# Performance work log

Hardware: AMD Instinct MI355X
Metric: run time of the kernel (lower is better)

Reference implementation:

```python
import jax, jax.numpy as jnp
import numpy as np

D_MODEL = 1024
NUM_HEADS = 16
HEAD_DIM = D_MODEL // NUM_HEADS  # 64
SCALE = HEAD_DIM ** -0.5
BIAS_LEN = 128  # min(max_seq_len=512, 128)
ROPE_BASE = 10000.0
LN_EPS = 1e-5


def setup_inputs() -> dict:
    key = jax.random.key(0)
    ks = jax.random.split(key, 8)
    B, Lq, Lkv = 8, 512, 512
    return {
        "decoder_hidden": jax.random.normal(ks[0], (B, Lq, D_MODEL), jnp.float32),
        "encoder_output": jax.random.normal(ks[1], (B, Lkv, D_MODEL), jnp.float32),
        "Wqkv": jax.random.normal(ks[2], (3 * D_MODEL, D_MODEL), jnp.float32) * 0.02,
        "Wout": jax.random.normal(ks[3], (D_MODEL, D_MODEL), jnp.float32) * 0.02,
        "b_out": jnp.zeros((D_MODEL,), jnp.float32),
        "Wgate": jax.random.normal(ks[4], (D_MODEL, D_MODEL), jnp.float32) * 0.02,
        "b_gate": jnp.zeros((D_MODEL,), jnp.float32),
        "gamma": jnp.ones((D_MODEL,), jnp.float32),
        "beta": jnp.zeros((D_MODEL,), jnp.float32),
    }


def _layernorm(x, gamma, beta):
    mu = jnp.mean(x, axis=-1, keepdims=True)
    var = jnp.mean(jnp.square(x - mu), axis=-1, keepdims=True)
    return (x - mu) * jax.lax.rsqrt(var + LN_EPS) * gamma + beta


def _rope(x, cos, sin):
    # x: [B, H, L, HEAD_DIM]; cos/sin: [L, HEAD_DIM//2]
    half = HEAD_DIM // 2
    c = cos[None, None, :, :]
    s = sin[None, None, :, :]
    x_even, x_odd = x[..., :half], x[..., half:]
    return jnp.concatenate([x_even * c - x_odd * s, x_even * s + x_odd * c], axis=-1)


def _temporal_bias(L_q, L_kv):
    pos = jnp.arange(BIAS_LEN, dtype=jnp.float32)
    dist = jnp.abs(pos[None, :] - pos[:, None])  # [128,128]
    bias = jnp.exp(-dist * 0.1) - dist * 0.05
    if L_q <= BIAS_LEN and L_kv <= BIAS_LEN:
        return bias[:L_q, :L_kv]
    # bilinear interpolation (align_corners=False / half-pixel) fallback
    return jax.image.resize(bias, (L_q, L_kv), method="bilinear")


def reference(decoder_hidden, encoder_output, Wqkv, Wout, b_out, Wgate, b_gate, gamma, beta):
    B, L_q, _ = decoder_hidden.shape
    L_kv = encoder_output.shape[1]
    residual = decoder_hidden

    q_in = _layernorm(decoder_hidden, gamma, beta)
    kv_in = _layernorm(encoder_output, gamma, beta)

    q = q_in @ Wqkv[:D_MODEL].T
    k = kv_in @ Wqkv[D_MODEL:2 * D_MODEL].T
    v = kv_in @ Wqkv[2 * D_MODEL:].T

    q = q.reshape(B, L_q, NUM_HEADS, HEAD_DIM).transpose(0, 2, 1, 3)
    k = k.reshape(B, L_kv, NUM_HEADS, HEAD_DIM).transpose(0, 2, 1, 3)
    v = v.reshape(B, L_kv, NUM_HEADS, HEAD_DIM).transpose(0, 2, 1, 3)

    # rotary embedding over max(L_q, L_kv) positions
    L = max(L_q, L_kv)
    inv_freq = 1.0 / ROPE_BASE ** (jnp.arange(0, HEAD_DIM, 2, dtype=jnp.float32) / HEAD_DIM)
    freqs = jnp.arange(L, dtype=jnp.float32)[:, None] * inv_freq[None, :]  # [L, HEAD_DIM//2]
    cos, sin = jnp.cos(freqs), jnp.sin(freqs)
    q = _rope(q, cos[:L_q], sin[:L_q])
    k = _rope(k, cos[:L_kv], sin[:L_kv])

    scores = jnp.einsum("bhqd,bhkd->bhqk", q, k) * SCALE
    scores = scores + _temporal_bias(L_q, L_kv)[None, None, :, :]

    attn = jax.nn.softmax(scores, axis=-1)
    attended = jnp.einsum("bhqk,bhkd->bhqd", attn, v)
    attended = attended.transpose(0, 2, 1, 3).reshape(B, L_q, D_MODEL)
    attended = attended @ Wout.T + b_out

    gate = jax.nn.sigmoid(attended @ Wgate.T + b_gate)
    output = gate * attended + (1.0 - gate) * residual
    return output
```

## Files before the change

kernel.cpp:

```cpp
#include <hip/hip_runtime.h>
#include <hip/hip_bf16.h>

#define D_MODEL 1024
#define NHEADS 16
#define HDIM 64
#define BATCH 8
#define SEQ 512
#define NROWS 4096
#define SCALE 0.125f
#define LN_EPS 1e-5f

typedef __attribute__((ext_vector_type(8))) short bf16x8;
typedef __attribute__((ext_vector_type(4))) float f32x4;
typedef __attribute__((ext_vector_type(8))) unsigned short u16x8;

static __device__ __forceinline__ float bf2f(unsigned short u) {
    return __uint_as_float(((unsigned int)u) << 16);
}
static __device__ __forceinline__ unsigned short f2bf(float f) {
    unsigned int x = __float_as_uint(f);
    unsigned int r = (x + 0x7fffu + ((x >> 16) & 1u)) >> 16;
    return (unsigned short)r;
}

#define GLOAD16(gp, lp)                                                        \
    __builtin_amdgcn_global_load_lds(                                          \
        (const __attribute__((address_space(1))) void*)(gp),                   \
        (__attribute__((address_space(3))) void*)(lp), 16, 0, 0)

#define VMW(n) asm volatile("s_waitcnt vmcnt(" #n ")" ::: "memory")
#define RBAR() __builtin_amdgcn_s_barrier()

static __device__ __forceinline__ float bias128(int a, int b) {
    float d = fabsf((float)(a - b));
    return expf(-d * 0.1f) - d * 0.05f;
}

__global__ void prep_kernel(const float* __restrict__ dec, const float* __restrict__ enc,
                            const float* __restrict__ gamma, const float* __restrict__ beta,
                            const float* __restrict__ Wqkv,
                            const float* __restrict__ Wout, const float* __restrict__ Wgate,
                            unsigned short* __restrict__ q_ln, unsigned short* __restrict__ kv_ln,
                            float* __restrict__ bias, unsigned short* __restrict__ Wqkv_bf,
                            unsigned short* __restrict__ Wout_bf, unsigned short* __restrict__ Wgate_bf) {
    int blk = blockIdx.x;
    int t = threadIdx.x;
    if (blk >= 12288) {
        int idx = (blk - 12288) * 256 + t;
        const float* src; unsigned short* dst; int off;
        if (idx < 262144) { src = Wout; dst = Wout_bf; off = idx; }
        else              { src = Wgate; dst = Wgate_bf; off = idx - 262144; }
        float4 v = ((const float4*)src)[off];
        ushort4 u;
        u.x = f2bf(v.x); u.y = f2bf(v.y); u.z = f2bf(v.z); u.w = f2bf(v.w);
        ((ushort4*)dst)[off] = u;
        return;
    }
    if (blk >= 9216) {
        int idx = (blk - 9216) * 256 + t;
        float4 v = ((const float4*)Wqkv)[idx];
        ushort4 u;
        u.x = f2bf(v.x); u.y = f2bf(v.y); u.z = f2bf(v.z); u.w = f2bf(v.w);
        ((ushort4*)Wqkv_bf)[idx] = u;
        return;
    }
    if (blk >= 8192) {
        int idx = (blk - 8192) * 256 + t;
        int qi = idx >> 9, kj = idx & 511;
        float fq = (qi + 0.5f) * 0.25f - 0.5f;
        float fk = (kj + 0.5f) * 0.25f - 0.5f;
        int iq = (int)floorf(fq); float tq = fq - (float)iq;
        int ik = (int)floorf(fk); float tk = fk - (float)ik;
        int iq0 = min(max(iq, 0), 127), iq1 = min(max(iq + 1, 0), 127);
        int ik0 = min(max(ik, 0), 127), ik1 = min(max(ik + 1, 0), 127);
        float v = (1.f - tq) * ((1.f - tk) * bias128(iq0, ik0) + tk * bias128(iq0, ik1))
                +        tq  * ((1.f - tk) * bias128(iq1, ik0) + tk * bias128(iq1, ik1));
        bias[idx] = v;
        return;
    }
    int row = blk;
    const float* src = (row < NROWS) ? dec + (size_t)row * D_MODEL
                                     : enc + (size_t)(row - NROWS) * D_MODEL;
    unsigned short* dst = (row < NROWS) ? q_ln + (size_t)row * D_MODEL
                                        : kv_ln + (size_t)(row - NROWS) * D_MODEL;
    float4 x = ((const float4*)src)[t];
    float s  = x.x + x.y + x.z + x.w;
    float ss = x.x * x.x + x.y * x.y + x.z * x.z + x.w * x.w;
    #pragma unroll
    for (int off = 32; off > 0; off >>= 1) {
        s  += __shfl_down(s, off);
        ss += __shfl_down(ss, off);
    }
    __shared__ float red_s[4], red_ss[4];
    int wid = t >> 6, lane = t & 63;
    if (lane == 0) { red_s[wid] = s; red_ss[wid] = ss; }
    __syncthreads();
    if (t == 0) {
        float S = red_s[0] + red_s[1] + red_s[2] + red_s[3];
        float SS = red_ss[0] + red_ss[1] + red_ss[2] + red_ss[3];
        red_s[0] = S; red_ss[0] = SS;
    }
    __syncthreads();
    float mu  = red_s[0] * (1.0f / 1024.0f);
    float var = red_ss[0] * (1.0f / 1024.0f) - mu * mu;
    float rstd = rsqrtf(var + LN_EPS);
    float4 g = ((const float4*)gamma)[t];
    float4 bb = ((const float4*)beta)[t];
    ushort4 u;
    u.x = f2bf((x.x - mu) * rstd * g.x + bb.x);
    u.y = f2bf((x.y - mu) * rstd * g.y + bb.y);
    u.z = f2bf((x.z - mu) * rstd * g.z + bb.z);
    u.w = f2bf((x.w - mu) * rstd * g.w + bb.w);
    ((ushort4*)dst)[t] = u;
}

__global__ void convert_og(const float* __restrict__ Wout, const float* __restrict__ Wgate,
                           unsigned short* __restrict__ Wout_bf, unsigned short* __restrict__ Wgate_bf) {
    int idx = blockIdx.x * 256 + threadIdx.x;
    const float* src; unsigned short* dst; int off;
    if (idx < 262144) { src = (const float*)Wout; dst = Wout_bf; off = idx; }
    else              { src = (const float*)Wgate; dst = Wgate_bf; off = idx - 262144; }
    float4 v = ((const float4*)src)[off];
    ushort4 u;
    u.x = f2bf(v.x); u.y = f2bf(v.y); u.z = f2bf(v.z); u.w = f2bf(v.w);
    ((ushort4*)dst)[off] = u;
}

#define CSTR 136

struct alignas(16) Smem64B {
    unsigned short A[64 * 128];
    unsigned short B[128 * 128];
};

#define MF(a, b, d) __builtin_amdgcn_mfma_f32_16x16x32_bf16((a), (b), (d), 0, 0, 0)

#define GEMM_KH2B(kh)                                                          \
    {                                                                          \
        int pofs = (((kh) * 4 + quad) ^ c) * 8;                                \
        const unsigned short* Arow_ = &As2[(wr * 32 + c) * 128 + pofs];        \
        const unsigned short* Brow_ = &Bs2[(wc * 64 + c) * 128 + pofs];        \
        bf16x8 f0 = *(const bf16x8*)(Arow_);                                   \
        bf16x8 f1 = *(const bf16x8*)(Arow_ + 2048);                            \
        bf16x8 g0 = *(const bf16x8*)(Brow_);                                   \
        bf16x8 g1 = *(const bf16x8*)(Brow_ + 2048);                            \
        bf16x8 g2 = *(const bf16x8*)(Brow_ + 4096);                            \
        bf16x8 g3 = *(const bf16x8*)(Brow_ + 6144);                            \
        c00 = MF(f0, g0, c00); c01 = MF(f0, g1, c01); c02 = MF(f0, g2, c02); c03 = MF(f0, g3, c03); \
        c10 = MF(f1, g0, c10); c11 = MF(f1, g1, c11); c12 = MF(f1, g2, c12); c13 = MF(f1, g3, c13); \
    }

#define GEMM_BODY_64B(Aptr, Bptr)                                              \
    int wave = tid >> 6, lane = tid & 63, quad = lane >> 4, c = lane & 15;     \
    int wr = wave >> 1, wc = wave & 1;                                         \
    int l4 = lane >> 4, l15 = lane & 15;                                       \
    const unsigned short* Abase = (Aptr) + (size_t)(rt * 64) * 1024;           \
    const unsigned short* Bbase = (Bptr) + (size_t)(ct * 128) * 1024;          \
    int aoff0 = (wave * 16 +  0 + l4) * 1024 + ((l15 ^ ( 0 + l4)) * 8);        \
    int aoff1 = (wave * 16 +  4 + l4) * 1024 + ((l15 ^ ( 4 + l4)) * 8);        \
    int aoff2 = (wave * 16 +  8 + l4) * 1024 + ((l15 ^ ( 8 + l4)) * 8);        \
    int aoff3 = (wave * 16 + 12 + l4) * 1024 + ((l15 ^ (12 + l4)) * 8);        \
    int boff0 = (wave * 32 +  0 + l4) * 1024 + ((l15 ^ (( 0 + l4) & 15)) * 8); \
    int boff1 = (wave * 32 +  4 + l4) * 1024 + ((l15 ^ (( 4 + l4) & 15)) * 8); \
    int boff2 = (wave * 32 +  8 + l4) * 1024 + ((l15 ^ (( 8 + l4) & 15)) * 8); \
    int boff3 = (wave * 32 + 12 + l4) * 1024 + ((l15 ^ ((12 + l4) & 15)) * 8); \
    int boff4 = (wave * 32 + 16 + l4) * 1024 + ((l15 ^ ((16 + l4) & 15)) * 8); \
    int boff5 = (wave * 32 + 20 + l4) * 1024 + ((l15 ^ ((20 + l4) & 15)) * 8); \
    int boff6 = (wave * 32 + 24 + l4) * 1024 + ((l15 ^ ((24 + l4) & 15)) * 8); \
    int boff7 = (wave * 32 + 28 + l4) * 1024 + ((l15 ^ ((28 + l4) & 15)) * 8); \
    unsigned short* AsW = As2 + wave * 2048;                                   \
    unsigned short* BsW = Bs2 + wave * 4096;                                   \
    f32x4 c00 = (f32x4)0.f, c01 = (f32x4)0.f, c02 = (f32x4)0.f, c03 = (f32x4)0.f; \
    f32x4 c10 = (f32x4)0.f, c11 = (f32x4)0.f, c12 = (f32x4)0.f, c13 = (f32x4)0.f; \
    for (int kt = 0; kt < 8; ++kt) {                                           \
        int k0 = kt * 128;                                                     \
        __syncthreads();                                                       \
        GLOAD16(Abase + aoff0 + k0, AsW);                                      \
        GLOAD16(Abase + aoff1 + k0, AsW + 512);                                \
        GLOAD16(Abase + aoff2 + k0, AsW + 1024);                               \
        GLOAD16(Abase + aoff3 + k0, AsW + 1536);                               \
        GLOAD16(Bbase + boff0 + k0, BsW);                                      \
        GLOAD16(Bbase + boff1 + k0, BsW + 512);                                \
        GLOAD16(Bbase + boff2 + k0, BsW + 1024);                               \
        GLOAD16(Bbase + boff3 + k0, BsW + 1536);                               \
        GLOAD16(Bbase + boff4 + k0, BsW + 2048);                               \
        GLOAD16(Bbase + boff5 + k0, BsW + 2560);                               \
        GLOAD16(Bbase + boff6 + k0, BsW + 3072);                               \
        GLOAD16(Bbase + boff7 + k0, BsW + 3584);                               \
        __syncthreads();                                                       \
        GEMM_KH2B(0)                                                           \
        GEMM_KH2B(1)                                                           \
        GEMM_KH2B(2)                                                           \
        GEMM_KH2B(3)                                                           \
    }

union alignas(16) SmemQS {
    struct { unsigned short A[64 * 64]; unsigned short B[128 * 64]; } ab;
    unsigned short C[64 * CSTR];
    unsigned short Ct[128 * 72];
};

#define QKH(pA, pB, kh)                                                        \
    {                                                                          \
        int pofs = (((kh) * 4 + quad) ^ x7) * 8;                               \
        const unsigned short* Ar_ = (pA) + (wr * 32 + c) * 64 + pofs;          \
        const unsigned short* Br_ = (pB) + (wc * 64 + c) * 64 + pofs;          \
        bf16x8 f0 = *(const bf16x8*)(Ar_);                                     \
        bf16x8 f1 = *(const bf16x8*)(Ar_ + 1024);                              \
        bf16x8 g0 = *(const bf16x8*)(Br_);                                     \
        bf16x8 g1 = *(const bf16x8*)(Br_ + 1024);                              \
        bf16x8 g2 = *(const bf16x8*)(Br_ + 2048);                              \
        bf16x8 g3 = *(const bf16x8*)(Br_ + 3072);                              \
        c00 = MF(f0, g0, c00); c01 = MF(f0, g1, c01); c02 = MF(f0, g2, c02); c03 = MF(f0, g3, c03); \
        c10 = MF(f1, g0, c10); c11 = MF(f1, g1, c11); c12 = MF(f1, g2, c12); c13 = MF(f1, g3, c13); \
    }

#define QROPE_REG(i, reg, A0, A1, A2, A3)                                      \
    {                                                                          \
        int mloc = wr * 32 + (i) * 16 + quad * 4 + (reg);                      \
        int crow = mloc * CSTR + wc * 64;                                      \
        float fl = (float)((rt * 64 + mloc) & 511);                            \
        float aa0 = fl * inv0, aa1 = fl * inv1;                                \
        float c0 = cosf(aa0), s0 = sinf(aa0);                                  \
        float c1 = cosf(aa1), s1 = sinf(aa1);                                  \
        float e0 = A0[(reg)], o0 = A2[(reg)];                                  \
        float e1 = A1[(reg)], o1 = A3[(reg)];                                  \
        smemq.C[crow + c]      = f2bf(e0 * c0 - o0 * s0);                      \
        smemq.C[crow + 32 + c] = f2bf(e0 * s0 + o0 * c0);                      \
        smemq.C[crow + 16 + c] = f2bf(e1 * c1 - o1 * s1);                      \
        smemq.C[crow + 48 + c] = f2bf(e1 * s1 + o1 * c1);                      \
    }
#define QROPE_ROW(i, A0, A1, A2, A3)                                           \
    QROPE_REG(i, 0, A0, A1, A2, A3) QROPE_REG(i, 1, A0, A1, A2, A3)            \
    QROPE_REG(i, 2, A0, A1, A2, A3) QROPE_REG(i, 3, A0, A1, A2, A3)

#define QVSECT_REG(i, j, reg, Acc)                                             \
    smemq.Ct[(wc * 64 + (j) * 16 + c) * 72 + (wr * 32 + (i) * 16 + quad * 4 + (reg))] = f2bf(Acc[(reg)]);
#define QVSECT_TILE(i, j, Acc)                                                 \
    QVSECT_REG(i, j, 0, Acc) QVSECT_REG(i, j, 1, Acc)                          \
    QVSECT_REG(i, j, 2, Acc) QVSECT_REG(i, j, 3, Acc)

__global__ __launch_bounds__(256, 6)
void qkv_gemm_mfma(const unsigned short* __restrict__ q_ln,
                   const unsigned short* __restrict__ kv_ln,
                   const unsigned short* __restrict__ Wb,
                   unsigned short* __restrict__ qo,
                   unsigned short* __restrict__ ko,
                   unsigned short* __restrict__ vo) {
    int bid = blockIdx.x;
    int wg = (bid & 7) * 192 + (bid >> 3);
    int st = wg >> 5, in = wg & 31;
    int stc = st >> 4, str = st & 15;
    int ct = stc * 8 + (in & 7);
    int rt = str * 4 + (in >> 3);
    int n0 = ct * 128;
    int section = stc;
    const unsigned short* A = (section == 0) ? q_ln : kv_ln;

    __shared__ SmemQS smemq;
    unsigned short* As2 = smemq.ab.A;
    unsigned short* Bs2 = smemq.ab.B;
    int tid = threadIdx.x;
    int wave = tid >> 6, lane = tid & 63, quad = lane >> 4, c = lane & 15;
    int wr = wave >> 1, wc = wave & 1;
    int x7 = c & 7;

    int soff = (tid >> 3) * 1024 + (((tid & 7) ^ ((tid >> 3) & 7)) * 8);
    const unsigned short* Ab = A + (size_t)(rt * 64) * 1024 + soff;
    const unsigned short* Bb = Wb + (size_t)n0 * 1024 + soff;
    int stW = wave * 512;

    f32x4 c00 = (f32x4)0.f, c01 = (f32x4)0.f, c02 = (f32x4)0.f, c03 = (f32x4)0.f;
    f32x4 c10 = (f32x4)0.f, c11 = (f32x4)0.f, c12 = (f32x4)0.f, c13 = (f32x4)0.f;

    for (int kt = 0; kt < 16; ++kt) {
        int k0 = kt * 64;
        __syncthreads();
        GLOAD16(Ab + k0,          As2 + stW);
        GLOAD16(Ab + 32768 + k0,  As2 + stW + 2048);
        GLOAD16(Bb + k0,          Bs2 + stW);
        GLOAD16(Bb + 32768 + k0,  Bs2 + stW + 2048);
        GLOAD16(Bb + 65536 + k0,  Bs2 + stW + 4096);
        GLOAD16(Bb + 98304 + k0,  Bs2 + stW + 6144);
        __syncthreads();
        QKH(As2, Bs2, 0)
        QKH(As2, Bs2, 1)
    }

    __syncthreads();

    if (section == 2) {
        QVSECT_TILE(0, 0, c00) QVSECT_TILE(0, 1, c01) QVSECT_TILE(0, 2, c02) QVSECT_TILE(0, 3, c03)
        QVSECT_TILE(1, 0, c10) QVSECT_TILE(1, 1, c11) QVSECT_TILE(1, 2, c12) QVSECT_TILE(1, 3, c13)
        __syncthreads();
        int dr = tid >> 1, hh = tid & 1;
        int h = ((n0 & 1023) >> 6) + (dr >> 6);
        int d = dr & 63;
        int mmb = rt * 64;
        int bb = mmb >> 9, ll0 = mmb & 511;
        unsigned short* orow = vo + (((size_t)bb * NHEADS + h) * HDIM + d) * SEQ + ll0 + hh * 32;
        const unsigned short* csrc = &smemq.Ct[dr * 72 + hh * 32];
        #pragma unroll
        for (int kc = 0; kc < 4; ++kc)
            *(u16x8*)(orow + kc * 8) = *(const u16x8*)(csrc + kc * 8);
        return;
    }

    float inv0 = expf(-0.2878231366f * (float)c);
    float inv1 = expf(-0.2878231366f * (float)(16 + c));
    QROPE_ROW(0, c00, c01, c02, c03)
    QROPE_ROW(1, c10, c11, c12, c13)
    __syncthreads();

    unsigned short* outp = (section == 0) ? qo : ko;
    int rr = tid >> 2;
    int ch = (tid >> 1) & 1;
    int sub = tid & 1;
    int mm = rt * 64 + rr;
    int bb = mm >> 9, ll = mm & 511;
    int h = ((n0 & 1023) >> 6) + ch;
    unsigned short* orow = outp + (((size_t)bb * NHEADS + h) * SEQ + ll) * HDIM + sub * 32;
    const unsigned short* csrc = &smemq.C[rr * CSTR + ch * 64 + sub * 32];
    #pragma unroll
    for (int kc = 0; kc < 4; ++kc)
        *(u16x8*)(orow + kc * 8) = *(const u16x8*)(csrc + kc * 8);
}

#define O1_REG(mb, reg, n, Acc)                                                \
    t_bf[(size_t)((mb) + (reg)) * 1024 + (n)] = f2bf(Acc[(reg)] + bo);
#define O1_TILE(i, j, Acc)                                                     \
    {                                                                          \
        int n = ct * 128 + wc * 64 + (j) * 16 + c;                             \
        float bo = b_out[n];                                                   \
        int mb = rt * 64 + wr * 32 + (i) * 16 + quad * 4;                      \
        O1_REG(mb, 0, n, Acc) O1_REG(mb, 1, n, Acc)                            \
        O1_REG(mb, 2, n, Acc) O1_REG(mb, 3, n, Acc)                            \
    }

__global__ __launch_bounds__(256, 1)
void out_gemm1_mfma(const unsigned short* __restrict__ att,
                    const unsigned short* __restrict__ Wob,
                    const float* __restrict__ b_out,
                    unsigned short* __restrict__ t_bf) {
    int ct = blockIdx.x, rt = blockIdx.y;
    __shared__ Smem64B smem2;
    unsigned short* As2 = smem2.A;
    unsigned short* Bs2 = smem2.B;
    int tid = threadIdx.x;

    GEMM_BODY_64B(att, Wob)

    O1_TILE(0, 0, c00) O1_TILE(0, 1, c01) O1_TILE(0, 2, c02) O1_TILE(0, 3, c03)
    O1_TILE(1, 0, c10) O1_TILE(1, 1, c11) O1_TILE(1, 2, c12) O1_TILE(1, 3, c13)
}

#define O2_REG(mb, reg, n, Acc)                                                \
    {                                                                          \
        float gz = Acc[(reg)] + bg;                                            \
        float g = 1.0f / (1.0f + expf(-gz));                                   \
        size_t idx = (size_t)((mb) + (reg)) * 1024 + (n);                      \
        float tv = bf2f(t_bf[idx]);                                            \
        float rv = residual[idx];                                              \
        out[idx] = g * tv + (1.0f - g) * rv;                                   \
    }
#define O2_TILE(i, j, Acc)                                                     \
    {                                                                          \
        int n = ct * 128 + wc * 64 + (j) * 16 + c;                             \
        float bg = b_gate[n];                                                  \
        int mb = rt * 64 + wr * 32 + (i) * 16 + quad * 4;                      \
        O2_REG(mb, 0, n, Acc) O2_REG(mb, 1, n, Acc)                            \
        O2_REG(mb, 2, n, Acc) O2_REG(mb, 3, n, Acc)                            \
    }

__global__ __launch_bounds__(256, 1)
void out_gemm2_mfma(const unsigned short* __restrict__ t_bf,
                    const unsigned short* __restrict__ Wgb,
                    const float* __restrict__ b_gate,
                    const float* __restrict__ residual,
                    float* __restrict__ out) {
    int ct = blockIdx.x, rt = blockIdx.y;
    __shared__ Smem64B smem2;
    unsigned short* As2 = smem2.A;
    unsigned short* Bs2 = smem2.B;
    int tid = threadIdx.x;

    GEMM_BODY_64B(t_bf, Wgb)

    O2_TILE(0, 0, c00) O2_TILE(0, 1, c01) O2_TILE(0, 2, c02) O2_TILE(0, 3, c03)
    O2_TILE(1, 0, c10) O2_TILE(1, 1, c11) O2_TILE(1, 2, c12) O2_TILE(1, 3, c13)
}

#define KSTR 72

static __device__ __forceinline__ void attn_step(
    const unsigned short* __restrict__ KsB, const unsigned short* __restrict__ VsB,
    int kv0, const float* __restrict__ bias, unsigned short* __restrict__ Ps,
    int q0, int wb, int quad, int c, int p0, int p1,
    bf16x8 aq0, bf16x8 aq1, f32x4 (&oacc)[4], float (&lrow)[4])
{
    f32x4 sacc[4];
    #pragma unroll
    for (int nt = 0; nt < 4; ++nt) {
        const unsigned short* kbase = &KsB[(nt * 16 + c) * 64];
        bf16x8 b0 = *(const bf16x8*)(kbase + p0);
        bf16x8 b1 = *(const bf16x8*)(kbase + p1);
        f32x4 a = (f32x4)0.f;
        a = __builtin_amdgcn_mfma_f32_16x16x32_bf16(aq0, b0, a, 0, 0, 0);
        a = __builtin_amdgcn_mfma_f32_16x16x32_bf16(aq1, b1, a, 0, 0, 0);
        sacc[nt] = a;
    }
    const float* bbase = bias + (size_t)(q0 + wb + quad * 4) * 512 + kv0 + c;
    float tsum[4];
    #pragma unroll
    for (int r = 0; r < 4; ++r) tsum[r] = 0.f;
    #pragma unroll
    for (int nt = 0; nt < 4; ++nt)
        #pragma unroll
        for (int r = 0; r < 4; ++r) {
            float p = __expf(sacc[nt][r] * SCALE + bbase[(size_t)r * 512 + nt * 16]);
            tsum[r] += p;
            Ps[(wb + quad * 4 + r) * KSTR + nt * 16 + c] = f2bf(p);
        }
    #pragma unroll
    for (int r = 0; r < 4; ++r) {
        float t = tsum[r];
        t += __shfl_xor(t, 1);
        t += __shfl_xor(t, 2);
        t += __shfl_xor(t, 4);
        t += __shfl_xor(t, 8);
        lrow[r] += t;
    }
    bf16x8 pb0 = *(const bf16x8*)&Ps[(wb + c) * KSTR + quad * 8];
    bf16x8 pb1 = *(const bf16x8*)&Ps[(wb + c) * KSTR + 32 + quad * 8];
    #pragma unroll
    for (int t = 0; t < 4; ++t) {
        const unsigned short* vbase = &VsB[(t * 16 + c) * 64];
        bf16x8 a0 = *(const bf16x8*)(vbase + p0);
        bf16x8 a1 = *(const bf16x8*)(vbase + p1);
        oacc[t] = __builtin_amdgcn_mfma_f32_16x16x32_bf16(a0, pb0, oacc[t], 0, 0, 0);
        oacc[t] = __builtin_amdgcn_mfma_f32_16x16x32_bf16(a1, pb1, oacc[t], 0, 0, 0);
    }
}

#define ASTAGE(BUF, kvt)                                                       \
    GLOAD16(kgb + (size_t)((kvt) * 64) * HDIM, Ks[BUF] + wave * 512);          \
    GLOAD16(vgb + (kvt) * 64, Vs[BUF] + wave * 512);

__global__ __launch_bounds__(512)
void attn_kernel(const unsigned short* __restrict__ q,
                 const unsigned short* __restrict__ k,
                 const unsigned short* __restrict__ vt,
                 const float* __restrict__ bias,
                 unsigned short* __restrict__ attended) {
    int qt = blockIdx.x, h = blockIdx.y, b = blockIdx.z;
    __shared__ unsigned short Ks[2][64 * 64];
    __shared__ unsigned short Vs[2][64 * 64];
    __shared__ unsigned short Ps[128 * KSTR];
    __shared__ float lf[128];

    int tid = threadIdx.x;
    int wave = tid >> 6, lane = tid & 63;
    int quad = lane >> 4, c = lane & 15;
    int wb = wave * 16;
    size_t headbase = (((size_t)b * NHEADS + h) * SEQ) * HDIM;
    int q0 = qt * 128;

    const unsigned short* qrow = q + headbase + (size_t)(q0 + wb + c) * HDIM;
    bf16x8 aq0 = *(const bf16x8*)(qrow + quad * 8);
    bf16x8 aq1 = *(const bf16x8*)(qrow + 32 + quad * 8);

    int srow = wave * 8 + (lane >> 3);
    int schunk = (lane & 7) ^ (srow & 7);
    const unsigned short* kgb = k + headbase + (size_t)srow * HDIM + schunk * 8;
    const unsigned short* vgb = vt + headbase + (size_t)srow * SEQ + schunk * 8;
    int x7 = c & 7;
    int p0 = (quad ^ x7) * 8;
    int p1 = ((4 + quad) ^ x7) * 8;

    f32x4 oacc[4];
    #pragma unroll
    for (int t = 0; t < 4; ++t) oacc[t] = (f32x4)0.f;
    float lrow[4];
    #pragma unroll
    for (int r = 0; r < 4; ++r) lrow[r] = 0.f;

    ASTAGE(0, 0)
    ASTAGE(1, 1)
    VMW(2); RBAR();
    for (int kt2 = 0; kt2 < 4; ++kt2) {
        attn_step(Ks[0], Vs[0], (kt2 * 2) * 64, bias, Ps,
                  q0, wb, quad, c, p0, p1, aq0, aq1, oacc, lrow);
        RBAR();
        if (kt2 < 3) { ASTAGE(0, kt2 * 2 + 2) VMW(2); }
        else         { VMW(0); }
        RBAR();
        attn_step(Ks[1], Vs[1], (kt2 * 2 + 1) * 64, bias, Ps,
                  q0, wb, quad, c, p0, p1, aq0, aq1, oacc, lrow);
        RBAR();
        if (kt2 < 3) { ASTAGE(1, kt2 * 2 + 3) VMW(2); }
        RBAR();
    }

    if (c == 0) {
        f32x4 lv;
        lv[0] = lrow[0]; lv[1] = lrow[1]; lv[2] = lrow[2]; lv[3] = lrow[3];
        *(f32x4*)&lf[wb + quad * 4] = lv;
    }
    float invl = 1.0f / lf[wb + c];
    unsigned short* drow = attended + ((size_t)b * SEQ + (q0 + wb + c)) * D_MODEL + h * HDIM;
    #pragma unroll
    for (int t = 0; t < 4; ++t) {
        ushort4 o;
        o.x = f2bf(oacc[t][0] * invl);
        o.y = f2bf(oacc[t][1] * invl);
        o.z = f2bf(oacc[t][2] * invl);
        o.w = f2bf(oacc[t][3] * invl);
        *(ushort4*)(drow + t * 16 + quad * 4) = o;
    }
}

extern "C" void kernel_launch(void* const* d_in, const int* in_sizes, int n_in,
                              void* d_out, int out_size, void* d_ws, size_t ws_size,
                              hipStream_t stream) {
    const float* dec    = (const float*)d_in[0];
    const float* enc    = (const float*)d_in[1];
    const float* Wqkv   = (const float*)d_in[2];
    const float* Wout   = (const float*)d_in[3];
    const float* b_out  = (const float*)d_in[4];
    const float* Wgate  = (const float*)d_in[5];
    const float* b_gate = (const float*)d_in[6];
    const float* gamma  = (const float*)d_in[7];
    const float* beta   = (const float*)d_in[8];
    float* out = (float*)d_out;

    char* ws = (char*)d_ws;
    const size_t MB = 1024 * 1024;
    unsigned short* q_ln    = (unsigned short*)(ws + 0 * MB);
    unsigned short* kv_ln   = (unsigned short*)(ws + 8 * MB);
    unsigned short* qb      = (unsigned short*)(ws + 16 * MB);
    unsigned short* kb      = (unsigned short*)(ws + 24 * MB);
    unsigned short* vb      = (unsigned short*)(ws + 32 * MB);
    unsigned short* Wqkv_bf = (unsigned short*)(ws + 40 * MB);
    float*          bias    = (float*)(ws + 46 * MB);
    unsigned short* att     = (unsigned short*)(ws + 0 * MB);
    unsigned short* t_bf    = (unsigned short*)(ws + 24 * MB);

    bool hoist = (ws_size >= 51 * MB);
    unsigned short* Wout_bf  = (unsigned short*)(ws + (hoist ? 47 * MB : 32 * MB));
    unsigned short* Wgate_bf = (unsigned short*)(ws + (hoist ? 49 * MB : 34 * MB));

    prep_kernel<<<hoist ? 14336 : 12288, 256, 0, stream>>>(
        dec, enc, gamma, beta, Wqkv, Wout, Wgate,
        q_ln, kv_ln, bias, Wqkv_bf, Wout_bf, Wgate_bf);
    qkv_gemm_mfma<<<1536, 256, 0, stream>>>(q_ln, kv_ln, Wqkv_bf, qb, kb, vb);
    attn_kernel<<<dim3(4, 16, 8), 512, 0, stream>>>(qb, kb, vb, bias, att);
    if (!hoist)
        convert_og<<<2048, 256, 0, stream>>>(Wout, Wgate, Wout_bf, Wgate_bf);
    out_gemm1_mfma<<<dim3(8, 64), 256, 0, stream>>>(att, Wout_bf, b_out, t_bf);
    out_gemm2_mfma<<<dim3(8, 64), 256, 0, stream>>>(t_bf, Wgate_bf, b_gate, dec, out);
}
```

Before: 207.8 us.

## Shrink output GEMM tiles to 64x64 with swizzled grid; one-wave-per-row layernorm

```diff
diff --git a/kernel.cpp b/kernel.cpp
--- a/kernel.cpp
+++ b/kernel.cpp
@@ -45,8 +45,8 @@
                             unsigned short* __restrict__ Wout_bf, unsigned short* __restrict__ Wgate_bf) {
     int blk = blockIdx.x;
     int t = threadIdx.x;
-    if (blk >= 12288) {
-        int idx = (blk - 12288) * 256 + t;
+    if (blk >= 6144) {
+        int idx = (blk - 6144) * 256 + t;
         const float* src; unsigned short* dst; int off;
         if (idx < 262144) { src = Wout; dst = Wout_bf; off = idx; }
         else              { src = Wgate; dst = Wgate_bf; off = idx - 262144; }
@@ -56,16 +56,16 @@
         ((ushort4*)dst)[off] = u;
         return;
     }
-    if (blk >= 9216) {
-        int idx = (blk - 9216) * 256 + t;
+    if (blk >= 3072) {
+        int idx = (blk - 3072) * 256 + t;
         float4 v = ((const float4*)Wqkv)[idx];
         ushort4 u;
         u.x = f2bf(v.x); u.y = f2bf(v.y); u.z = f2bf(v.z); u.w = f2bf(v.w);
         ((ushort4*)Wqkv_bf)[idx] = u;
         return;
     }
-    if (blk >= 8192) {
-        int idx = (blk - 8192) * 256 + t;
+    if (blk >= 2048) {
+        int idx = (blk - 2048) * 256 + t;
         int qi = idx >> 9, kj = idx & 511;
         float fq = (qi + 0.5f) * 0.25f - 0.5f;
         float fk = (kj + 0.5f) * 0.25f - 0.5f;
@@ -78,40 +78,44 @@
         bias[idx] = v;
         return;
     }
-    int row = blk;
+    int row = blk * 4 + (t >> 6);
+    int lane = t & 63;
     const float* src = (row < NROWS) ? dec + (size_t)row * D_MODEL
                                      : enc + (size_t)(row - NROWS) * D_MODEL;
     unsigned short* dst = (row < NROWS) ? q_ln + (size_t)row * D_MODEL
                                         : kv_ln + (size_t)(row - NROWS) * D_MODEL;
-    float4 x = ((const float4*)src)[t];
-    float s  = x.x + x.y + x.z + x.w;
-    float ss = x.x * x.x + x.y * x.y + x.z * x.z + x.w * x.w;
+    float4 x0 = ((const float4*)src)[lane];
+    float4 x1 = ((const float4*)src)[lane + 64];
+    float4 x2 = ((const float4*)src)[lane + 128];
+    float4 x3 = ((const float4*)src)[lane + 192];
+    float s  = x0.x + x0.y + x0.z + x0.w + x1.x + x1.y + x1.z + x1.w
+             + x2.x + x2.y + x2.z + x2.w + x3.x + x3.y + x3.z + x3.w;
+    float ss = x0.x * x0.x + x0.y * x0.y + x0.z * x0.z + x0.w * x0.w
+             + x1.x * x1.x + x1.y * x1.y + x1.z * x1.z + x1.w * x1.w
+             + x2.x * x2.x + x2.y * x2.y + x2.z * x2.z + x2.w * x2.w
+             + x3.x * x3.x + x3.y * x3.y + x3.z * x3.z + x3.w * x3.w;
     #pragma unroll
     for (int off = 32; off > 0; off >>= 1) {
         s  += __shfl_down(s, off);
         ss += __shfl_down(ss, off);
     }
-    __shared__ float red_s[4], red_ss[4];
-    int wid = t >> 6, lane = t & 63;
-    if (lane == 0) { red_s[wid] = s; red_ss[wid] = ss; }
-    __syncthreads();
-    if (t == 0) {
-        float S = red_s[0] + red_s[1] + red_s[2] + red_s[3];
-        float SS = red_ss[0] + red_ss[1] + red_ss[2] + red_ss[3];
-        red_s[0] = S; red_ss[0] = SS;
-    }
-    __syncthreads();
-    float mu  = red_s[0] * (1.0f / 1024.0f);
-    float var = red_ss[0] * (1.0f / 1024.0f) - mu * mu;
+    s  = __shfl(s, 0);
+    ss = __shfl(ss, 0);
+    float mu  = s * (1.0f / 1024.0f);
+    float var = ss * (1.0f / 1024.0f) - mu * mu;
     float rstd = rsqrtf(var + LN_EPS);
-    float4 g = ((const float4*)gamma)[t];
-    float4 bb = ((const float4*)beta)[t];
-    ushort4 u;
-    u.x = f2bf((x.x - mu) * rstd * g.x + bb.x);
-    u.y = f2bf((x.y - mu) * rstd * g.y + bb.y);
-    u.z = f2bf((x.z - mu) * rstd * g.z + bb.z);
-    u.w = f2bf((x.w - mu) * rstd * g.w + bb.w);
-    ((ushort4*)dst)[t] = u;
+    #pragma unroll
+    for (int j = 0; j < 4; ++j) {
+        float4 xv = (j == 0) ? x0 : (j == 1) ? x1 : (j == 2) ? x2 : x3;
+        float4 g  = ((const float4*)gamma)[lane + j * 64];
+        float4 bb = ((const float4*)beta)[lane + j * 64];
+        ushort4 u;
+        u.x = f2bf((xv.x - mu) * rstd * g.x + bb.x);
+        u.y = f2bf((xv.y - mu) * rstd * g.y + bb.y);
+        u.z = f2bf((xv.z - mu) * rstd * g.z + bb.z);
+        u.w = f2bf((xv.w - mu) * rstd * g.w + bb.w);
+        ((ushort4*)dst)[lane + j * 64] = u;
+    }
 }
 
 __global__ void convert_og(const float* __restrict__ Wout, const float* __restrict__ Wgate,
@@ -128,71 +132,7 @@
 
 #define CSTR 136
 
-struct alignas(16) Smem64B {
-    unsigned short A[64 * 128];
-    unsigned short B[128 * 128];
-};
-
 #define MF(a, b, d) __builtin_amdgcn_mfma_f32_16x16x32_bf16((a), (b), (d), 0, 0, 0)
-
-#define GEMM_KH2B(kh)                                                          \
-    {                                                                          \
-        int pofs = (((kh) * 4 + quad) ^ c) * 8;                                \
-        const unsigned short* Arow_ = &As2[(wr * 32 + c) * 128 + pofs];        \
-        const unsigned short* Brow_ = &Bs2[(wc * 64 + c) * 128 + pofs];        \
-        bf16x8 f0 = *(const bf16x8*)(Arow_);                                   \
-        bf16x8 f1 = *(const bf16x8*)(Arow_ + 2048);                            \
-        bf16x8 g0 = *(const bf16x8*)(Brow_);                                   \
-        bf16x8 g1 = *(const bf16x8*)(Brow_ + 2048);                            \
-        bf16x8 g2 = *(const bf16x8*)(Brow_ + 4096);                            \
-        bf16x8 g3 = *(const bf16x8*)(Brow_ + 6144);                            \
-        c00 = MF(f0, g0, c00); c01 = MF(f0, g1, c01); c02 = MF(f0, g2, c02); c03 = MF(f0, g3, c03); \
-        c10 = MF(f1, g0, c10); c11 = MF(f1, g1, c11); c12 = MF(f1, g2, c12); c13 = MF(f1, g3, c13); \
-    }
-
-#define GEMM_BODY_64B(Aptr, Bptr)                                              \
-    int wave = tid >> 6, lane = tid & 63, quad = lane >> 4, c = lane & 15;     \
-    int wr = wave >> 1, wc = wave & 1;                                         \
-    int l4 = lane >> 4, l15 = lane & 15;                                       \
-    const unsigned short* Abase = (Aptr) + (size_t)(rt * 64) * 1024;           \
-    const unsigned short* Bbase = (Bptr) + (size_t)(ct * 128) * 1024;          \
-    int aoff0 = (wave * 16 +  0 + l4) * 1024 + ((l15 ^ ( 0 + l4)) * 8);        \
-    int aoff1 = (wave * 16 +  4 + l4) * 1024 + ((l15 ^ ( 4 + l4)) * 8);        \
-    int aoff2 = (wave * 16 +  8 + l4) * 1024 + ((l15 ^ ( 8 + l4)) * 8);        \
-    int aoff3 = (wave * 16 + 12 + l4) * 1024 + ((l15 ^ (12 + l4)) * 8);        \
-    int boff0 = (wave * 32 +  0 + l4) * 1024 + ((l15 ^ (( 0 + l4) & 15)) * 8); \
-    int boff1 = (wave * 32 +  4 + l4) * 1024 + ((l15 ^ (( 4 + l4) & 15)) * 8); \
-    int boff2 = (wave * 32 +  8 + l4) * 1024 + ((l15 ^ (( 8 + l4) & 15)) * 8); \
-    int boff3 = (wave * 32 + 12 + l4) * 1024 + ((l15 ^ ((12 + l4) & 15)) * 8); \
-    int boff4 = (wave * 32 + 16 + l4) * 1024 + ((l15 ^ ((16 + l4) & 15)) * 8); \
-    int boff5 = (wave * 32 + 20 + l4) * 1024 + ((l15 ^ ((20 + l4) & 15)) * 8); \
-    int boff6 = (wave * 32 + 24 + l4) * 1024 + ((l15 ^ ((24 + l4) & 15)) * 8); \
-    int boff7 = (wave * 32 + 28 + l4) * 1024 + ((l15 ^ ((28 + l4) & 15)) * 8); \
-    unsigned short* AsW = As2 + wave * 2048;                                   \
-    unsigned short* BsW = Bs2 + wave * 4096;                                   \
-    f32x4 c00 = (f32x4)0.f, c01 = (f32x4)0.f, c02 = (f32x4)0.f, c03 = (f32x4)0.f; \
-    f32x4 c10 = (f32x4)0.f, c11 = (f32x4)0.f, c12 = (f32x4)0.f, c13 = (f32x4)0.f; \
-    for (int kt = 0; kt < 8; ++kt) {                                           \
-        int k0 = kt * 128;                                                     \
-        __syncthreads();                                                       \
-        GLOAD16(Abase + aoff0 + k0, AsW);                                      \
-        GLOAD16(Abase + aoff1 + k0, AsW + 512);                                \
-        GLOAD16(Abase + aoff2 + k0, AsW + 1024);                               \
-        GLOAD16(Abase + aoff3 + k0, AsW + 1536);                               \
-        GLOAD16(Bbase + boff0 + k0, BsW);                                      \
-        GLOAD16(Bbase + boff1 + k0, BsW + 512);                                \
-        GLOAD16(Bbase + boff2 + k0, BsW + 1024);                               \
-        GLOAD16(Bbase + boff3 + k0, BsW + 1536);                               \
-        GLOAD16(Bbase + boff4 + k0, BsW + 2048);                               \
-        GLOAD16(Bbase + boff5 + k0, BsW + 2560);                               \
-        GLOAD16(Bbase + boff6 + k0, BsW + 3072);                               \
-        GLOAD16(Bbase + boff7 + k0, BsW + 3584);                               \
-        __syncthreads();                                                       \
-        GEMM_KH2B(0)                                                           \
-        GEMM_KH2B(1)                                                           \
-        GEMM_KH2B(2)                                                           \
-        GEMM_KH2B(3)                                                           \
-    }
 
 union alignas(16) SmemQS {
     struct { unsigned short A[64 * 64]; unsigned short B[128 * 64]; } ab;
@@ -326,32 +266,70 @@
         *(u16x8*)(orow + kc * 8) = *(const u16x8*)(csrc + kc * 8);
 }
 
+struct alignas(16) SmemOG {
+    unsigned short A[64 * 64];
+    unsigned short B[64 * 64];
+};
+
+#define OG_KH(kh)                                                              \
+    {                                                                          \
+        int pofs = (((kh) * 4 + quad) ^ x7) * 8;                               \
+        const unsigned short* Ar_ = smemog.A + (wr * 32 + c) * 64 + pofs;      \
+        const unsigned short* Br_ = smemog.B + (wc * 32 + c) * 64 + pofs;      \
+        bf16x8 f0 = *(const bf16x8*)(Ar_);                                     \
+        bf16x8 f1 = *(const bf16x8*)(Ar_ + 1024);                              \
+        bf16x8 g0 = *(const bf16x8*)(Br_);                                     \
+        bf16x8 g1 = *(const bf16x8*)(Br_ + 1024);                              \
+        c00 = MF(f0, g0, c00); c01 = MF(f0, g1, c01);                          \
+        c10 = MF(f1, g0, c10); c11 = MF(f1, g1, c11);                          \
+    }
+
+#define OG_BODY(Aptr, Bptr)                                                    \
+    int bid = blockIdx.x;                                         \
+    int wg = (bid & 7) * 128 + (bid >> 3);      \
+    int ct = wg & 15, rt = wg >> 4;                                            \
+    int tid = threadIdx.x;                                                     \
+    int wave = tid >> 6, lane = tid & 63, quad = lane >> 4, c = lane & 15;     \
+    int wr = wave >> 1, wc = wave & 1;                                         \
+    int x7 = c & 7;                                                            \
+    int soff = (tid >> 3) * 1024 + (((tid & 7) ^ ((tid >> 3) & 7)) * 8);       \
+    const unsigned short* Ab = (Aptr) + (size_t)(rt * 64) * 1024 + soff;       \
+    const unsigned short* Bb = (Bptr) + (size_t)(ct * 64) * 1024 + soff;       \
+    int stW = wave * 512;                                                      \
+    f32x4 c00 = (f32x4)0.f, c01 = (f32x4)0.f;                                  \
+    f32x4 c10 = (f32x4)0.f, c11 = (f32x4)0.f;                                  \
+    for (int kt = 0; kt < 16; ++kt) {                                          \
+        int k0 = kt * 64;                                                      \
+        __syncthreads();                                                       \
+        GLOAD16(Ab + k0,          smemog.A + stW);                             \
+        GLOAD16(Ab + 32768 + k0,  smemog.A + stW + 2048);                      \
+        GLOAD16(Bb + k0,          smemog.B + stW);                             \
+        GLOAD16(Bb + 32768 + k0,  smemog.B + stW + 2048);                      \
+        __syncthreads();                                                       \
+        OG_KH(0)                                                               \
+        OG_KH(1)                                                               \
+    }
+
 #define O1_REG(mb, reg, n, Acc)                                                \
     t_bf[(size_t)((mb) + (reg)) * 1024 + (n)] = f2bf(Acc[(reg)] + bo);
 #define O1_TILE(i, j, Acc)                                                     \
     {                                                                          \
-        int n = ct * 128 + wc * 64 + (j) * 16 + c;                             \
+        int n = ct * 64 + wc * 32 + (j) * 16 + c;                              \
         float bo = b_out[n];                                                   \
         int mb = rt * 64 + wr * 32 + (i) * 16 + quad * 4;                      \
         O1_REG(mb, 0, n, Acc) O1_REG(mb, 1, n, Acc)                            \
         O1_REG(mb, 2, n, Acc) O1_REG(mb, 3, n, Acc)                            \
     }
 
-__global__ __launch_bounds__(256, 1)
+__global__ __launch_bounds__(256, 4)
 void out_gemm1_mfma(const unsigned short* __restrict__ att,
                     const unsigned short* __restrict__ Wob,
                     const float* __restrict__ b_out,
                     unsigned short* __restrict__ t_bf) {
-    int ct = blockIdx.x, rt = blockIdx.y;
-    __shared__ Smem64B smem2;
-    unsigned short* As2 = smem2.A;
-    unsigned short* Bs2 = smem2.B;
-    int tid = threadIdx.x;
-
-    GEMM_BODY_64B(att, Wob)
-
-    O1_TILE(0, 0, c00) O1_TILE(0, 1, c01) O1_TILE(0, 2, c02) O1_TILE(0, 3, c03)
-    O1_TILE(1, 0, c10) O1_TILE(1, 1, c11) O1_TILE(1, 2, c12) O1_TILE(1, 3, c13)
+    __shared__ SmemOG smemog;
+    OG_BODY(att, Wob)
+    O1_TILE(0, 0, c00) O1_TILE(0, 1, c01)
+    O1_TILE(1, 0, c10) O1_TILE(1, 1, c11)
 }
 
 #define O2_REG(mb, reg, n, Acc)                                                \
@@ -365,29 +343,23 @@
     }
 #define O2_TILE(i, j, Acc)                                                     \
     {                                                                          \
-        int n = ct * 128 + wc * 64 + (j) * 16 + c;                             \
+        int n = ct * 64 + wc * 32 + (j) * 16 + c;                              \
         float bg = b_gate[n];                                                  \
         int mb = rt * 64 + wr * 32 + (i) * 16 + quad * 4;                      \
         O2_REG(mb, 0, n, Acc) O2_REG(mb, 1, n, Acc)                            \
         O2_REG(mb, 2, n, Acc) O2_REG(mb, 3, n, Acc)                            \
     }
 
-__global__ __launch_bounds__(256, 1)
+__global__ __launch_bounds__(256, 4)
 void out_gemm2_mfma(const unsigned short* __restrict__ t_bf,
                     const unsigned short* __restrict__ Wgb,
                     const float* __restrict__ b_gate,
                     const float* __restrict__ residual,
                     float* __restrict__ out) {
-    int ct = blockIdx.x, rt = blockIdx.y;
-    __shared__ Smem64B smem2;
-    unsigned short* As2 = smem2.A;
-    unsigned short* Bs2 = smem2.B;
-    int tid = threadIdx.x;
-
-    GEMM_BODY_64B(t_bf, Wgb)
-
-    O2_TILE(0, 0, c00) O2_TILE(0, 1, c01) O2_TILE(0, 2, c02) O2_TILE(0, 3, c03)
-    O2_TILE(1, 0, c10) O2_TILE(1, 1, c11) O2_TILE(1, 2, c12) O2_TILE(1, 3, c13)
+    __shared__ SmemOG smemog;
+    OG_BODY(t_bf, Wgb)
+    O2_TILE(0, 0, c00) O2_TILE(0, 1, c01)
+    O2_TILE(1, 0, c10) O2_TILE(1, 1, c11)
 }
 
 #define KSTR 72
@@ -549,13 +521,13 @@
     unsigned short* Wout_bf  = (unsigned short*)(ws + (hoist ? 47 * MB : 32 * MB));
     unsigned short* Wgate_bf = (unsigned short*)(ws + (hoist ? 49 * MB : 34 * MB));
 
-    prep_kernel<<<hoist ? 14336 : 12288, 256, 0, stream>>>(
+    prep_kernel<<<hoist ? 8192 : 6144, 256, 0, stream>>>(
         dec, enc, gamma, beta, Wqkv, Wout, Wgate,
         q_ln, kv_ln, bias, Wqkv_bf, Wout_bf, Wgate_bf);
     qkv_gemm_mfma<<<1536, 256, 0, stream>>>(q_ln, kv_ln, Wqkv_bf, qb, kb, vb);
     attn_kernel<<<dim3(4, 16, 8), 512, 0, stream>>>(qb, kb, vb, bias, att);
     if (!hoist)
         convert_og<<<2048, 256, 0, stream>>>(Wout, Wgate, Wout_bf, Wgate_bf);
-    out_gemm1_mfma<<<dim3(8, 64), 256, 0, stream>>>(att, Wout_bf, b_out, t_bf);
-    out_gemm2_mfma<<<dim3(8, 64), 256, 0, stream>>>(t_bf, Wgate_bf, b_gate, dec, out);
-}
+    out_gemm1_mfma<<<1024, 256, 0, stream>>>(att, Wout_bf, b_out, t_bf);
+    out_gemm2_mfma<<<1024, 256, 0, stream>>>(t_bf, Wgate_bf, b_gate, dec, out);
+}
```

Measured after the change: 203.1 us. 1.02x faster.
